# Performance work log

Measured on AMD Instinct MI355X. Metric: run time of the kernel, lower is better.

Reference implementation:

```python
import jax, jax.numpy as jnp
import numpy as np

N = 50000       # nodes
E = 800000      # edges
D_IN, D_H, D_OUT = 64, 64, 32


def _glorot(key, fan_in, fan_out):
    lim = np.sqrt(6.0 / (fan_in + fan_out)).astype(np.float32)
    return jax.random.uniform(key, (fan_in, fan_out), jnp.float32, -lim, lim)


def setup_inputs() -> dict:
    key = jax.random.key(0)
    k = jax.random.split(key, 4)
    x = jax.random.normal(k[0], (N, D_IN), jnp.float32)
    edge_index = jax.random.randint(k[1], (2, E), 0, N, dtype=jnp.int64)
    W1 = _glorot(k[2], D_IN, D_H)
    b1 = jnp.zeros((D_H,), jnp.float32)
    W2 = _glorot(k[3], D_H, D_OUT)
    b2 = jnp.zeros((D_OUT,), jnp.float32)
    return {"x": x, "edge_index": edge_index, "W1": W1, "b1": b1, "W2": W2, "b2": b2}


def gcn_layer(x, W, b, src, dst, n):
    # PyG GCNConv: h = XW; add self-loops (weight 1); symmetric normalization
    # out[j] = sum_{i->j} h[i] / sqrt(deg(i) deg(j)) + h[j]/deg(j) + b
    h = x @ W                                           # [n, d_out]
    deg = jax.ops.segment_sum(jnp.ones((src.shape[0],), h.dtype), dst,
                              num_segments=n) + 1.0     # in-degree + self-loop
    dinv = jax.lax.rsqrt(deg)                           # deg >= 1
    norm = (dinv[src] * dinv[dst])[:, None]             # [E, 1]
    agg = jax.ops.segment_sum(h[src] * norm, dst, num_segments=n)
    # self-loop contribution: dinv[i]*dinv[i]*h[i]
    return agg + h * (dinv * dinv)[:, None] + b


def reference(x, edge_index, W1, b1, W2, b2):
    src, dst = edge_index[0], edge_index[1]
    h = gcn_layer(x, W1, b1, src, dst, N)
    h = jax.nn.relu(h)                                  # dropout is identity in eval mode
    return gcn_layer(h, W2, b2, src, dst, N)
```

## Files before the change

### kernel.cpp

```cpp
#include <hip/hip_runtime.h>
#include <hip/hip_fp16.h>
#include <cstddef>
#include <cstdint>

namespace {

constexpr int N  = 50000;
constexpr int E  = 800000;
constexpr int DH = 64;
constexpr int DO = 32;
constexpr int NB = (N + 255) / 256;
static_assert(N < 65536, "src packed as u16");
static_assert(NB <= 256, "phase-B single tile");

__device__ inline float bf2f(uint16_t u) {
    union { uint32_t u; float f; } c; c.u = (uint32_t)u << 16; return c.f;
}
__device__ inline uint16_t f2bf(float f) {
    union { float f; uint32_t u; } c; c.f = f;
    uint32_t r = c.u + 0x7FFFu + ((c.u >> 16) & 1u);
    return (uint16_t)(r >> 16);
}
__device__ inline void bf2x(uint32_t p, float& a, float& b) {
    union { uint32_t u; float f; } c0, c1;
    c0.u = p << 16; c1.u = p & 0xFFFF0000u;
    a = c0.f; b = c1.f;
}

__global__ void k_zero(int* __restrict__ cnt) {
    int i = blockIdx.x * blockDim.x + threadIdx.x;
    if (i < N) cnt[i] = 0;
}

__global__ void k_count(const int* __restrict__ dst, int* __restrict__ cnt,
                        int* __restrict__ rank) {
    int e = blockIdx.x * blockDim.x + threadIdx.x;
    if (e < E) rank[e] = atomicAdd(&cnt[dst[e]], 1);
}

__global__ void k_scanA(const int* __restrict__ cnt, int* __restrict__ incl,
                        int* __restrict__ bsum) {
    __shared__ int ts[256];
    const int t = threadIdx.x;
    const int i = blockIdx.x * 256 + t;
    const int v = (i < N) ? cnt[i] : 0;
    ts[t] = v;
    __syncthreads();
#pragma unroll
    for (int off = 1; off < 256; off <<= 1) {
        const int u = (t >= off) ? ts[t - off] : 0;
        __syncthreads();
        ts[t] += u;
        __syncthreads();
    }
    if (i < N) incl[i] = ts[t];
    if (t == 255) bsum[blockIdx.x] = ts[255];
}

__global__ void k_scanB(int* __restrict__ bsum) {
    __shared__ int ts[256];
    const int t = threadIdx.x;
    const int v = (t < NB) ? bsum[t] : 0;
    ts[t] = v;
    __syncthreads();
#pragma unroll
    for (int off = 1; off < 256; off <<= 1) {
        const int u = (t >= off) ? ts[t - off] : 0;
        __syncthreads();
        ts[t] += u;
        __syncthreads();
    }
    if (t < NB) bsum[t] = ts[t] - v;
}

__global__ void k_scanC(const int* __restrict__ cnt, const int* __restrict__ incl,
                        const int* __restrict__ bbase, int* __restrict__ rowptr,
                        float* __restrict__ dinv) {
    const int i = blockIdx.x * 256 + threadIdx.x;
    if (i >= N) return;
    const int c    = cnt[i];
    const int excl = bbase[blockIdx.x] + incl[i] - c;
    rowptr[i] = excl;
    dinv[i]   = rsqrtf((float)(c + 1));
    if (i == N - 1) rowptr[N] = excl + c;
}

__global__ void k_fill(const int* __restrict__ src, const int* __restrict__ dst,
                       const int* __restrict__ rank, const int* __restrict__ rowptr,
                       const float* __restrict__ dinv, uint32_t* __restrict__ epack) {
    int e = blockIdx.x * blockDim.x + threadIdx.x;
    if (e >= E) return;
    const int s = src[e], d = dst[e];
    const int pos = rowptr[d] + rank[e];
    const float wn = dinv[s] * dinv[d];
    const uint16_t hb = __half_as_ushort(__float2half(wn));
    epack[pos] = (uint32_t)s | ((uint32_t)hb << 16);
}

template <int DOUT, typename OutT>
__global__ void k_gemm(const float* __restrict__ X, const float* __restrict__ W,
                       OutT* __restrict__ H) {
    __shared__ float Ws[64 * DOUT];
    const int tid = threadIdx.x;
    for (int i = tid; i < 64 * DOUT; i += 256) Ws[i] = W[i];
    __syncthreads();

    constexpr int RPI = 256 / DOUT;
    const int col  = tid % DOUT;
    const int rsub = tid / DOUT;
    const int rowBase = blockIdx.x * 64;

    for (int r0 = 0; r0 < 64; r0 += RPI) {
        const int row = rowBase + r0 + rsub;
        if (row < N) {
            const float4* xr4 = reinterpret_cast<const float4*>(X + (size_t)row * 64);
            float acc = 0.0f;
#pragma unroll
            for (int k4 = 0; k4 < 16; ++k4) {
                float4 xv = xr4[k4];
                acc += xv.x * Ws[(4 * k4 + 0) * DOUT + col];
                acc += xv.y * Ws[(4 * k4 + 1) * DOUT + col];
                acc += xv.z * Ws[(4 * k4 + 2) * DOUT + col];
                acc += xv.w * Ws[(4 * k4 + 3) * DOUT + col];
            }
            if constexpr (sizeof(OutT) == 2)
                H[(size_t)row * DOUT + col] = f2bf(acc);
            else
                H[(size_t)row * DOUT + col] = acc;
        }
    }
}

__global__ void k_agg1(const int* __restrict__ rowptr, const uint32_t* __restrict__ epack,
                       const uint16_t* __restrict__ h1, const float* __restrict__ dinv,
                       const float* __restrict__ b1, float* __restrict__ y1) {
    const int gtid = blockIdx.x * blockDim.x + threadIdx.x;
    const int n    = gtid >> 6;
    const int lane = gtid & 63;
    if (n >= N) return;
    const int g  = lane >> 3;
    const int sl = lane & 7;
    const int beg = rowptr[n], end = rowptr[n + 1];

    float acc[8] = {0.f, 0.f, 0.f, 0.f, 0.f, 0.f, 0.f, 0.f};
    for (int j = beg; j < end; j += 8) {
        const int jj = j + g;
        int s = 0; float wn = 0.0f;
        if (jj < end) {
            const uint32_t w = epack[jj];
            s  = (int)(w & 0xFFFFu);
            wn = __half2float(__ushort_as_half((uint16_t)(w >> 16)));
        }
        const uint4 v = *reinterpret_cast<const uint4*>(h1 + (size_t)s * DH + sl * 8);
        float f0, f1;
        bf2x(v.x, f0, f1); acc[0] += wn * f0; acc[1] += wn * f1;
        bf2x(v.y, f0, f1); acc[2] += wn * f0; acc[3] += wn * f1;
        bf2x(v.z, f0, f1); acc[4] += wn * f0; acc[5] += wn * f1;
        bf2x(v.w, f0, f1); acc[6] += wn * f0; acc[7] += wn * f1;
    }
#pragma unroll
    for (int m = 8; m < 64; m <<= 1)
#pragma unroll
        for (int k = 0; k < 8; ++k) acc[k] += __shfl_xor(acc[k], m);

    if (g < 2) {
        const float di = dinv[n], d2 = di * di;
        const int fb = sl * 8 + g * 4;
        const uint2 sv = *reinterpret_cast<const uint2*>(h1 + (size_t)n * DH + fb);
        float s0, s1, s2, s3;
        bf2x(sv.x, s0, s1); bf2x(sv.y, s2, s3);
        const float4 bv = *reinterpret_cast<const float4*>(b1 + fb);
        float4 o;
        o.x = fmaxf(acc[g * 4 + 0] + s0 * d2 + bv.x, 0.f);
        o.y = fmaxf(acc[g * 4 + 1] + s1 * d2 + bv.y, 0.f);
        o.z = fmaxf(acc[g * 4 + 2] + s2 * d2 + bv.z, 0.f);
        o.w = fmaxf(acc[g * 4 + 3] + s3 * d2 + bv.w, 0.f);
        *reinterpret_cast<float4*>(y1 + (size_t)n * DH + fb) = o;
    }
}

__global__ void k_agg2(const int* __restrict__ rowptr, const uint32_t* __restrict__ epack,
                       const float* __restrict__ h2, const float* __restrict__ dinv,
                       const float* __restrict__ b2, float* __restrict__ out) {
    const int gtid = blockIdx.x * blockDim.x + threadIdx.x;
    const int n    = gtid >> 6;
    const int lane = gtid & 63;
    if (n >= N) return;
    const int g  = lane >> 3;
    const int sl = lane & 7;
    const int beg = rowptr[n], end = rowptr[n + 1];

    float acc[4] = {0.f, 0.f, 0.f, 0.f};
    for (int j = beg; j < end; j += 8) {
        const int jj = j + g;
        int s = 0; float wn = 0.0f;
        if (jj < end) {
            const uint32_t w = epack[jj];
            s  = (int)(w & 0xFFFFu);
            wn = __half2float(__ushort_as_half((uint16_t)(w >> 16)));
        }
        const float4 v = *reinterpret_cast<const float4*>(h2 + (size_t)s * DO + sl * 4);
        acc[0] += wn * v.x; acc[1] += wn * v.y;
        acc[2] += wn * v.z; acc[3] += wn * v.w;
    }
#pragma unroll
    for (int m = 8; m < 64; m <<= 1)
#pragma unroll
        for (int k = 0; k < 4; ++k) acc[k] += __shfl_xor(acc[k], m);

    if (g == 0) {
        const float di = dinv[n], d2 = di * di;
        const float4 sv = *reinterpret_cast<const float4*>(h2 + (size_t)n * DO + sl * 4);
        const float4 bv = *reinterpret_cast<const float4*>(b2 + sl * 4);
        float4 o;
        o.x = acc[0] + sv.x * d2 + bv.x;
        o.y = acc[1] + sv.y * d2 + bv.y;
        o.z = acc[2] + sv.z * d2 + bv.z;
        o.w = acc[3] + sv.w * d2 + bv.w;
        *reinterpret_cast<float4*>(out + (size_t)n * DO + sl * 4) = o;
    }
}

template <typename T>
T* alignp(char*& p, size_t count) {
    uintptr_t u = ((uintptr_t)p + 63) & ~(uintptr_t)63;
    p = (char*)(u + count * sizeof(T));
    return (T*)u;
}

}

extern "C" void kernel_launch(void* const* d_in, const int* in_sizes, int n_in,
                              void* d_out, int out_size, void* d_ws, size_t ws_size,
                              hipStream_t stream) {
    const float* x   = (const float*)d_in[0];
    const int*   ei  = (const int*)d_in[1];
    const float* W1  = (const float*)d_in[2];
    const float* b1  = (const float*)d_in[3];
    const float* W2  = (const float*)d_in[4];
    const float* b2  = (const float*)d_in[5];
    float* out = (float*)d_out;

    const int* src = ei;
    const int* dst = ei + E;

    char* p = (char*)d_ws;
    int*      cnt    = alignp<int>(p, N);
    int*      rowptr = alignp<int>(p, N + 1);
    int*      rank   = alignp<int>(p, E);
    float*    dinv   = alignp<float>(p, N);
    int*      incl   = alignp<int>(p, N);
    int*      bsum   = alignp<int>(p, NB);
    uint32_t* epack  = alignp<uint32_t>(p, E);
    uint16_t* h1     = alignp<uint16_t>(p, (size_t)N * DH);
    float*    y1     = alignp<float>(p, (size_t)N * DH);
    float*    h2     = (float*)h1;

    hipLaunchKernelGGL(k_zero, dim3((N + 255) / 256), dim3(256), 0, stream, cnt);
    hipLaunchKernelGGL(k_count, dim3((E + 255) / 256), dim3(256), 0, stream,
                       dst, cnt, rank);
    hipLaunchKernelGGL(k_scanA, dim3(NB), dim3(256), 0, stream, cnt, incl, bsum);
    hipLaunchKernelGGL(k_scanB, dim3(1), dim3(256), 0, stream, bsum);
    hipLaunchKernelGGL(k_scanC, dim3(NB), dim3(256), 0, stream, cnt, incl, bsum,
                       rowptr, dinv);
    hipLaunchKernelGGL(k_fill, dim3((E + 255) / 256), dim3(256), 0, stream,
                       src, dst, rank, rowptr, dinv, epack);
    hipLaunchKernelGGL((k_gemm<DH, uint16_t>), dim3((N + 63) / 64), dim3(256), 0, stream,
                       x, W1, h1);
    hipLaunchKernelGGL(k_agg1, dim3((N * 64 + 255) / 256), dim3(256), 0, stream,
                       rowptr, epack, h1, dinv, b1, y1);
    hipLaunchKernelGGL((k_gemm<DO, float>), dim3((N + 63) / 64), dim3(256), 0, stream,
                       y1, W2, h2);
    hipLaunchKernelGGL(k_agg2, dim3((N * 64 + 255) / 256), dim3(256), 0, stream,
                       rowptr, epack, h2, dinv, b2, out);
}
```

Before: 177.0 us.

## Register-tile dense GEMM with shared-memory X staging and vectorized stores

Rewrites the node-feature GEMM so that each thread computes a 4-row by 2- or 4-column register tile. The 64x64 X tile is staged in padded shared memory and weights are loaded with float4, which cuts the per-FMA shared and global load traffic of the old one-output-per-thread loop. Output is written as packed bf16 uint2 or float2 vectors. The cost is more registers and extra LDS for the X tile, and the GEMM is only a small part of the whole pipeline.

Result: faster. 160.0 us (-9.6%).

```diff
diff --git a/kernel.cpp b/kernel.cpp
--- a/kernel.cpp
+++ b/kernel.cpp
@@ -98,35 +98,83 @@
 }
 
 template <int DOUT, typename OutT>
+__launch_bounds__(256)
 __global__ void k_gemm(const float* __restrict__ X, const float* __restrict__ W,
                        OutT* __restrict__ H) {
+    constexpr int CPT = DOUT / 16;
+    static_assert(CPT == 4 || CPT == 2, "geometry");
+    constexpr int XS = 68;
     __shared__ float Ws[64 * DOUT];
+    __shared__ float Xs[64 * XS];
+
     const int tid = threadIdx.x;
-    for (int i = tid; i < 64 * DOUT; i += 256) Ws[i] = W[i];
+    const int rowBase = blockIdx.x * 64;
+
+    constexpr int WF4 = 64 * DOUT / 4;
+#pragma unroll
+    for (int i = 0; i < WF4 / 256; ++i) {
+        const int q = tid + i * 256;
+        reinterpret_cast<float4*>(Ws)[q] = reinterpret_cast<const float4*>(W)[q];
+    }
+#pragma unroll
+    for (int i = 0; i < 4; ++i) {
+        const int q   = tid + i * 256;
+        const int row = q >> 4;
+        const int kq  = q & 15;
+        const int gr  = min(rowBase + row, N - 1);
+        const float4 v = *reinterpret_cast<const float4*>(X + (size_t)gr * 64 + kq * 4);
+        *reinterpret_cast<float4*>(&Xs[row * XS + kq * 4]) = v;
+    }
     __syncthreads();
 
-    constexpr int RPI = 256 / DOUT;
-    const int col  = tid % DOUT;
-    const int rsub = tid / DOUT;
-    const int rowBase = blockIdx.x * 64;
-
-    for (int r0 = 0; r0 < 64; r0 += RPI) {
-        const int row = rowBase + r0 + rsub;
+    const int rg = tid >> 4;
+    const int cg = tid & 15;
+
+    float acc[4][CPT];
+#pragma unroll
+    for (int r = 0; r < 4; ++r)
+#pragma unroll
+        for (int c = 0; c < CPT; ++c) acc[r][c] = 0.0f;
+
+#pragma unroll
+    for (int k4 = 0; k4 < 16; ++k4) {
+        const int k = k4 * 4;
+        float xr[4][4];
+#pragma unroll
+        for (int r = 0; r < 4; ++r) {
+            const float4 v = *reinterpret_cast<const float4*>(&Xs[(rg * 4 + r) * XS + k]);
+            xr[r][0] = v.x; xr[r][1] = v.y; xr[r][2] = v.z; xr[r][3] = v.w;
+        }
+#pragma unroll
+        for (int i = 0; i < 4; ++i) {
+            float wv[CPT];
+            if constexpr (CPT == 4) {
+                const float4 v = *reinterpret_cast<const float4*>(&Ws[(k + i) * DOUT + cg * 4]);
+                wv[0] = v.x; wv[1] = v.y; wv[2] = v.z; wv[3] = v.w;
+            } else {
+                const float2 v = *reinterpret_cast<const float2*>(&Ws[(k + i) * DOUT + cg * 2]);
+                wv[0] = v.x; wv[1] = v.y;
+            }
+#pragma unroll
+            for (int r = 0; r < 4; ++r)
+#pragma unroll
+                for (int c = 0; c < CPT; ++c) acc[r][c] += xr[r][i] * wv[c];
+        }
+    }
+
+#pragma unroll
+    for (int r = 0; r < 4; ++r) {
+        const int row = rowBase + rg * 4 + r;
         if (row < N) {
-            const float4* xr4 = reinterpret_cast<const float4*>(X + (size_t)row * 64);
-            float acc = 0.0f;
-#pragma unroll
-            for (int k4 = 0; k4 < 16; ++k4) {
-                float4 xv = xr4[k4];
-                acc += xv.x * Ws[(4 * k4 + 0) * DOUT + col];
-                acc += xv.y * Ws[(4 * k4 + 1) * DOUT + col];
-                acc += xv.z * Ws[(4 * k4 + 2) * DOUT + col];
-                acc += xv.w * Ws[(4 * k4 + 3) * DOUT + col];
+            if constexpr (sizeof(OutT) == 2) {
+                uint2 o;
+                o.x = (uint32_t)f2bf(acc[r][0]) | ((uint32_t)f2bf(acc[r][1]) << 16);
+                o.y = (uint32_t)f2bf(acc[r][2]) | ((uint32_t)f2bf(acc[r][3]) << 16);
+                *reinterpret_cast<uint2*>(&H[(size_t)row * DOUT + cg * 4]) = o;
+            } else {
+                float2 o; o.x = acc[r][0]; o.y = acc[r][1];
+                *reinterpret_cast<float2*>(&H[(size_t)row * DOUT + cg * 2]) = o;
             }
-            if constexpr (sizeof(OutT) == 2)
-                H[(size_t)row * DOUT + col] = f2bf(acc);
-            else
-                H[(size_t)row * DOUT + col] = acc;
         }
     }
 }
```
